# Optimization experiments

Measured on AMD Instinct MI355X. Metric: run time of the kernel, lower is better.

The kernel has to match this reference:

```python
import jax, jax.numpy as jnp
import numpy as np

HEADS = 8
EPS = 1e-5


def dwconv(x, w):
    # x: [B, C, L], w: [C, 1, K] depthwise kernel (groups == C), 'same' padding (K odd)
    K = w.shape[-1]
    p = (K - 1) // 2
    return jax.lax.conv_general_dilated(
        x, w, window_strides=(1,), padding=[(p, p)],
        dimension_numbers=('NCH', 'OIH', 'NCH'),
        feature_group_count=x.shape[1])


def dds_conv(x, pw, dw3, dw15, gate):
    # DynamicDepthSeparableConv1d: 1x1 pointwise (no bias) -> two depthwise convs
    # combined with softmax-gated weighted sum.
    o = jnp.einsum('oc,bcl->bol', pw, x)
    g = jax.nn.softmax(gate)
    return g[0] * dwconv(o, dw3) + g[1] * dwconv(o, dw15)


def instance_norm(x, gamma, beta):
    # InstanceNorm1d(affine=True), biased variance over length dim
    m = jnp.mean(x, axis=-1, keepdims=True)
    v = jnp.mean((x - m) ** 2, axis=-1, keepdims=True)
    return (x - m) * jax.lax.rsqrt(v + EPS) * gamma[None, :, None] + beta[None, :, None]


def block(x, p):
    B, C, L = x.shape
    h = HEADS
    Q = dds_conv(x, p['pw_q'], p['dw3_q'], p['dw15_q'], p['gate_q']).reshape(B, h, C, L)
    K = dds_conv(x, p['pw_k'], p['dw3_k'], p['dw15_k'], p['gate_k']).reshape(B, h, C, L)
    V = dds_conv(x, p['pw_v'], p['dw3_v'], p['dw15_v'], p['gate_v']).reshape(B, h, C, L)
    scale = C ** -0.25
    # dot[b,h,k,q] = sum_c K[b,h,c,k] * Q[b,h,c,q]; softmax over key dim (axis=2)
    dot = jnp.einsum('bhck,bhcq->bhkq', K * scale, Q * scale)
    attn = jax.nn.softmax(dot, axis=2)
    o = jnp.einsum('bhck,bhkq->bhcq', V, attn).reshape(B, h * C, L)
    attended = jnp.einsum('oc,bcl->bol', p['uni_W'], o) + p['uni_b'][None, :, None]
    # dropout is identity at inference
    x = instance_norm(attended + x, p['n1_g'], p['n1_b'])
    h1 = jax.nn.relu(jnp.einsum('oc,bcl->bol', p['ffn_W1'], x) + p['ffn_b1'][None, :, None])
    ff = jnp.einsum('oc,bcl->bol', p['ffn_W2'], h1) + p['ffn_b2'][None, :, None]
    x = instance_norm(ff + x, p['n2_g'], p['n2_b'])
    return x


def setup_inputs() -> dict:
    key = jax.random.key(0)
    ks = jax.random.split(key, 32)
    D, C, h, L, B, IN = 6, 32, HEADS, 2048, 8, 6
    CH = C * h
    s = 0.05
    inp = {
        'x': jax.random.normal(ks[0], (B, IN, L), jnp.float32),
        'enc_W': jax.random.normal(ks[1], (C, IN), jnp.float32) * s,
        'enc_b': jnp.zeros((C,), jnp.float32),
        'pw_q': jax.random.normal(ks[2], (D, CH, C), jnp.float32) * s,
        'dw3_q': jax.random.normal(ks[3], (D, CH, 1, 3), jnp.float32) * s,
        'dw15_q': jax.random.normal(ks[4], (D, CH, 1, 15), jnp.float32) * s,
        'gate_q': jnp.ones((D, 2), jnp.float32),
        'pw_k': jax.random.normal(ks[5], (D, CH, C), jnp.float32) * s,
        'dw3_k': jax.random.normal(ks[6], (D, CH, 1, 3), jnp.float32) * s,
        'dw15_k': jax.random.normal(ks[7], (D, CH, 1, 15), jnp.float32) * s,
        'gate_k': jnp.ones((D, 2), jnp.float32),
        'pw_v': jax.random.normal(ks[8], (D, CH, C), jnp.float32) * s,
        'dw3_v': jax.random.normal(ks[9], (D, CH, 1, 3), jnp.float32) * s,
        'dw15_v': jax.random.normal(ks[10], (D, CH, 1, 15), jnp.float32) * s,
        'gate_v': jnp.ones((D, 2), jnp.float32),
        'uni_W': jax.random.normal(ks[11], (D, C, CH), jnp.float32) * s,
        'uni_b': jnp.zeros((D, C), jnp.float32),
        'n1_g': jnp.ones((D, C), jnp.float32),
        'n1_b': jnp.zeros((D, C), jnp.float32),
        'n2_g': jnp.ones((D, C), jnp.float32),
        'n2_b': jnp.zeros((D, C), jnp.float32),
        'ffn_W1': jax.random.normal(ks[12], (D, 4 * C, C), jnp.float32) * s,
        'ffn_b1': jnp.zeros((D, 4 * C), jnp.float32),
        'ffn_W2': jax.random.normal(ks[13], (D, C, 4 * C), jnp.float32) * s,
        'ffn_b2': jnp.zeros((D, C), jnp.float32),
        'cls_W': jax.random.normal(ks[14], (1, C), jnp.float32) * s,
        'cls_b': jnp.zeros((1,), jnp.float32),
    }
    return inp


def reference(x, enc_W, enc_b, pw_q, dw3_q, dw15_q, gate_q, pw_k, dw3_k, dw15_k,
              gate_k, pw_v, dw3_v, dw15_v, gate_v, uni_W, uni_b, n1_g, n1_b,
              n2_g, n2_b, ffn_W1, ffn_b1, ffn_W2, ffn_b2, cls_W, cls_b):
    h = jnp.einsum('oc,bcl->bol', enc_W, x) + enc_b[None, :, None]
    params = dict(pw_q=pw_q, dw3_q=dw3_q, dw15_q=dw15_q, gate_q=gate_q,
                  pw_k=pw_k, dw3_k=dw3_k, dw15_k=dw15_k, gate_k=gate_k,
                  pw_v=pw_v, dw3_v=dw3_v, dw15_v=dw15_v, gate_v=gate_v,
                  uni_W=uni_W, uni_b=uni_b, n1_g=n1_g, n1_b=n1_b,
                  n2_g=n2_g, n2_b=n2_b, ffn_W1=ffn_W1, ffn_b1=ffn_b1,
                  ffn_W2=ffn_W2, ffn_b2=ffn_b2)
    def step(carry, p):
        return block(carry, p), None
    h, _ = jax.lax.scan(step, h, params)
    logits = jnp.einsum('oc,bcl->bol', cls_W, h) + cls_b[None, :, None]  # [B,1,L]
    return jax.nn.sigmoid(logits)[:, 0, :]  # strong (per-timestep) probabilities [B, L]
```

## Files before the change

### kernel.cpp

```cpp
#include <hip/hip_runtime.h>
#include <math.h>

#define LL   2048
#define BB   8
#define CC   32
#define CHH  256
#define HH   8
#define DD   6

typedef _Float16 h8 __attribute__((ext_vector_type(8)));
typedef _Float16 h4 __attribute__((ext_vector_type(4)));
typedef float f4 __attribute__((ext_vector_type(4)));
typedef float f2v __attribute__((ext_vector_type(2)));

__global__ __launch_bounds__(256) void k_enc(const float* __restrict__ x,
    const float* __restrict__ W, const float* __restrict__ bias,
    float* __restrict__ X) {
  int idx = blockIdx.x * 256 + threadIdx.x;
  int l = idx & (LL - 1);
  int c = (idx >> 11) & 31;
  int b = idx >> 16;
  float s = bias[c];
#pragma unroll
  for (int i = 0; i < 6; ++i)
    s = fmaf(W[c * 6 + i], x[((size_t)b * 6 + i) * LL + l], s);
  X[idx] = s;
}

__global__ __launch_bounds__(256) void k_qkv(const float* __restrict__ X,
    const float* __restrict__ pwq, const float* __restrict__ pwk,
    const float* __restrict__ pwv,
    const float* __restrict__ d3q, const float* __restrict__ d15q, const float* __restrict__ gq,
    const float* __restrict__ d3k, const float* __restrict__ d15k, const float* __restrict__ gk,
    const float* __restrict__ d3v, const float* __restrict__ d15v, const float* __restrict__ gv,
    _Float16* __restrict__ Qt, _Float16* __restrict__ Kt, _Float16* __restrict__ Vt) {
  __shared__ __align__(16) char lds[21504];
  int z  = blockIdx.y;
  int bx = blockIdx.x;
  int bh = bx >> 4, lt = bx & 15, l0 = lt * 128;
  int b = bh >> 3, h = bh & 7;
  int t = threadIdx.x;
  const float* pwp  = (z == 0) ? pwq  : (z == 1) ? pwk  : pwv;
  const float* w3p  = (z == 0) ? d3q  : (z == 1) ? d3k  : d3v;
  const float* w15p = (z == 0) ? d15q : (z == 1) ? d15k : d15v;
  const float* gp   = (z == 0) ? gq   : (z == 1) ? gk   : gv;

  char* Xh = lds;
  char* Wh = lds + 9728;
  char* ot = lds + 11776;

  {
    int r = t >> 3, u = t & 7;
    const float* xr = X + ((size_t)b * CC + r) * LL;
    char* xd = Xh + r * 304;
#pragma unroll
    for (int s = u; s < 36; s += 8) {
      int ls = l0 - 8 + s * 4;
      f4 v;
      if (ls >= 0 && ls + 3 < LL) {
        v = *(const f4*)(xr + ls);
      } else {
#pragma unroll
        for (int e = 0; e < 4; ++e) {
          int l = ls + e;
          v[e] = (l >= 0 && l < LL) ? xr[l] : 0.f;
        }
      }
      uint2 pk;
      pk.x = __builtin_bit_cast(unsigned, __builtin_amdgcn_cvt_pkrtz(v[0], v[1]));
      pk.y = __builtin_bit_cast(unsigned, __builtin_amdgcn_cvt_pkrtz(v[2], v[3]));
      *(uint2*)(xd + s * 8) = pk;
    }
  }
  {
    f4 wg = ((const f4*)(pwp + h * 1024))[t];
    uint2 pk;
    pk.x = __builtin_bit_cast(unsigned, __builtin_amdgcn_cvt_pkrtz(wg[0], wg[1]));
    pk.y = __builtin_bit_cast(unsigned, __builtin_amdgcn_cvt_pkrtz(wg[2], wg[3]));
    *(uint2*)(Wh + (t >> 3) * 64 + (t & 7) * 8) = pk;
  }
  __syncthreads();

  {
    int w4 = t >> 6, lane = t & 63;
    int g = lane >> 4, ln = lane & 15;
    h8 af[2];
#pragma unroll
    for (int mt = 0; mt < 2; ++mt)
      af[mt] = *(const h8*)(Wh + (mt * 16 + ln) * 64 + g * 16);
    for (int nt = w4; nt < 9; nt += 4) {
      h8 bf;
#pragma unroll
      for (int j = 0; j < 8; ++j)
        bf[j] = *(const _Float16*)(Xh + (g * 8 + j) * 304 + (nt * 16 + ln) * 2);
#pragma unroll
      for (int mt = 0; mt < 2; ++mt) {
        f4 zr = {0.f, 0.f, 0.f, 0.f};
        f4 d = __builtin_amdgcn_mfma_f32_16x16x32_f16(af[mt], bf, zr, 0, 0, 0);
#pragma unroll
        for (int i = 0; i < 4; ++i)
          *(_Float16*)(ot + (mt * 16 + g * 4 + i) * 304 + (nt * 16 + ln) * 2) =
              (_Float16)d[i];
      }
    }
  }
  __syncthreads();

  int c = t & 31, cg = t >> 5;
  float wv[32];
  {
    const h8* wp = (const h8*)(ot + c * 304 + cg * 32);
#pragma unroll
    for (int q4 = 0; q4 < 4; ++q4) {
      h8 v = wp[q4];
#pragma unroll
      for (int e = 0; e < 8; ++e) wv[q4 * 8 + e] = (float)v[e];
    }
  }
  float r0 = gp[0], r1 = gp[1];
  float mx = fmaxf(r0, r1);
  float e0 = __expf(r0 - mx), e1 = __expf(r1 - mx);
  float gi = 1.f / (e0 + e1);
  float g0 = e0 * gi, g1 = e1 * gi;
  float sc = (z == 0) ? 0.2550765737f : 1.0f;
  int ch = h * 32 + c;
  float w3r[3], w15r[15];
#pragma unroll
  for (int k = 0; k < 3; ++k)  w3r[k]  = w3p[ch * 3 + k];
#pragma unroll
  for (int k = 0; k < 15; ++k) w15r[k] = w15p[ch * 15 + k];

  h8 olo, ohi;
#pragma unroll
  for (int i = 0; i < 16; ++i) {
    float a = 0.f;
#pragma unroll
    for (int k = 0; k < 3; ++k) a = fmaf(w3r[k], wv[i + 7 + k], a);
    float s15 = 0.f;
#pragma unroll
    for (int k = 0; k < 15; ++k) s15 = fmaf(w15r[k], wv[i + 1 + k], s15);
    float val = (g0 * a + g1 * s15) * sc;
    if (i < 8) olo[i] = (_Float16)val; else ohi[i - 8] = (_Float16)val;
  }

  if (z == 2) {
    _Float16* dst = Vt + ((size_t)bh * 32 + c) * LL + l0 + cg * 16;
    *(h8*)dst = olo;
    *(h8*)(dst + 8) = ohi;
  } else {
    char* tb = lds;
    __syncthreads();
#pragma unroll
    for (int i = 0; i < 16; ++i) {
      _Float16 v = (i < 8) ? olo[i] : ohi[i - 8];
      *(_Float16*)(tb + (cg * 16 + i) * 80 + c * 2) = v;
    }
    __syncthreads();
    _Float16* dst = ((z == 0) ? Qt : Kt) + ((size_t)bh * LL + l0) * 32;
    int l = t >> 1, hf = t & 1;
    uint4 a = *(uint4*)(tb + l * 80 + hf * 32);
    uint4 b2 = *(uint4*)(tb + l * 80 + hf * 32 + 16);
    *(uint4*)(dst + (size_t)l * 32 + hf * 16) = a;
    *(uint4*)(dst + (size_t)l * 32 + hf * 16 + 8) = b2;
  }
}

__global__ __launch_bounds__(512, 2) void k_attn(
    const _Float16* __restrict__ Qt, const _Float16* __restrict__ Kt,
    const _Float16* __restrict__ Vt, _Float16* __restrict__ AO) {
  __shared__ __align__(16) char lds[38912];
  const int tid  = threadIdx.x;
  const int lane = tid & 63;
  const int w    = tid >> 6;
  const int seg  = w >> 2;
  const int wq   = w & 3;
  const int g    = lane >> 4;
  const int ln   = lane & 15;
  const int h2c  = (wq >> 1) * 2;
  const int lin  = blockIdx.x + (blockIdx.y << 4);
  const int swz  = ((lin & 7) << 7) | (lin >> 3);
  const int qb   = swz & 15;
  const int bh   = swz >> 4;
  const _Float16* Qg = Qt + ((size_t)bh * LL + qb * 128) * 32;
  const _Float16* Kg = Kt + ((size_t)bh * LL + seg * 1024) * 32;
  const _Float16* Vg = Vt + (size_t)bh * 32 * LL + seg * 1024;

  h8 qf[2];
#pragma unroll
  for (int nt = 0; nt < 2; ++nt)
    qf[nt] = *(const h8*)(Qg + (size_t)(wq * 32 + nt * 16 + ln) * 32 + g * 8);

  h8 ones;
#pragma unroll
  for (int j = 0; j < 8; ++j) ones[j] = (_Float16)1.0f;

  char* kb = lds + seg * 5120;
  char* vb = lds + 20480 + seg * 4608;

  uint4 stg0, stg1;
  if ((wq & 1) == 0) {
    const uint4* gk = (const uint4*)Kg;
    stg0 = gk[h2c * 64 + lane];
    stg1 = gk[(h2c + 1) * 64 + lane];
    *(uint4*)(kb + (h2c * 16 + (lane >> 2)) * 80 + (lane & 3) * 16) = stg0;
    *(uint4*)(kb + ((h2c + 1) * 16 + (lane >> 2)) * 80 + (lane & 3) * 16) = stg1;
  } else {
    int c0 = h2c * 8 + (lane >> 3);
    stg0 = *(const uint4*)(Vg + (size_t)c0 * LL + (lane & 7) * 8);
    stg1 = *(const uint4*)(Vg + (size_t)(c0 + 8) * LL + (lane & 7) * 8);
    *(uint4*)(vb + c0 * 144 + (lane & 7) * 16) = stg0;
    *(uint4*)(vb + (c0 + 8) * 144 + (lane & 7) * 16) = stg1;
  }
  __syncthreads();

  f4 o[2][2];
#pragma unroll
  for (int ct = 0; ct < 2; ++ct)
#pragma unroll
    for (int nt = 0; nt < 2; ++nt) o[ct][nt] = (f4){0.f, 0.f, 0.f, 0.f};
  f4 sacc[2];
#pragma unroll
  for (int nt = 0; nt < 2; ++nt) sacc[nt] = (f4){0.f, 0.f, 0.f, 0.f};

  for (int it = 0; it < 16; ++it) {
    int pp = it & 1;
    char* kbc = kb + pp * 10240;
    char* vbc = vb + pp * 9216;
    if (it < 15) {
      int k0n = (it + 1) * 64;
      if ((wq & 1) == 0) {
        const uint4* gk = (const uint4*)(Kg + (size_t)k0n * 32);
        stg0 = gk[h2c * 64 + lane];
        stg1 = gk[(h2c + 1) * 64 + lane];
      } else {
        int c0 = h2c * 8 + (lane >> 3);
        stg0 = *(const uint4*)(Vg + (size_t)c0 * LL + k0n + (lane & 7) * 8);
        stg1 = *(const uint4*)(Vg + (size_t)(c0 + 8) * LL + k0n + (lane & 7) * 8);
      }
    }
#pragma unroll
    for (int chunk = 0; chunk < 2; ++chunk) {
      unsigned pa[2][2], pb[2][2];
#pragma unroll
      for (int mt2 = 0; mt2 < 2; ++mt2) {
        h8 kf = *(const h8*)(kbc + ((chunk * 2 + mt2) * 16 + ln) * 80 + g * 16);
#pragma unroll
        for (int nt = 0; nt < 2; ++nt) {
          f4 z = {0.f, 0.f, 0.f, 0.f};
          f4 s = __builtin_amdgcn_mfma_f32_16x16x32_f16(kf, qf[nt], z, 0, 0, 0);
          float p0 = __builtin_amdgcn_exp2f(s[0]);
          float p1 = __builtin_amdgcn_exp2f(s[1]);
          float p2 = __builtin_amdgcn_exp2f(s[2]);
          float p3 = __builtin_amdgcn_exp2f(s[3]);
          unsigned lo = __builtin_bit_cast(unsigned,
              __builtin_amdgcn_cvt_pkrtz(p0, p1));
          unsigned hi = __builtin_bit_cast(unsigned,
              __builtin_amdgcn_cvt_pkrtz(p2, p3));
          if (mt2 == 0) { pa[nt][0] = lo; pa[nt][1] = hi; }
          else          { pb[nt][0] = lo; pb[nt][1] = hi; }
        }
      }
      h8 vf[2];
#pragma unroll
      for (int ct = 0; ct < 2; ++ct)
        vf[ct] = *(const h8*)(vbc + (ct * 16 + ln) * 144 + chunk * 64 + g * 16);
#pragma unroll
      for (int nt = 0; nt < 2; ++nt) {
        unsigned w0 = pa[nt][0], w1 = pa[nt][1];
        unsigned w2 = pb[nt][0], w3 = pb[nt][1];
        asm("v_permlane32_swap_b32 %0, %1" : "+v"(w0), "+v"(w2));
        asm("v_permlane16_swap_b32 %0, %1" : "+v"(w0), "+v"(w2));
        asm("v_permlane32_swap_b32 %0, %1" : "+v"(w1), "+v"(w3));
        asm("v_permlane16_swap_b32 %0, %1" : "+v"(w1), "+v"(w3));
        uint4 pw4; pw4.x = w0; pw4.y = w1; pw4.z = w2; pw4.w = w3;
        h8 pf = __builtin_bit_cast(h8, pw4);
        sacc[nt] = __builtin_amdgcn_mfma_f32_16x16x32_f16(ones, pf, sacc[nt], 0, 0, 0);
        o[0][nt] = __builtin_amdgcn_mfma_f32_16x16x32_f16(vf[0], pf, o[0][nt], 0, 0, 0);
        o[1][nt] = __builtin_amdgcn_mfma_f32_16x16x32_f16(vf[1], pf, o[1][nt], 0, 0, 0);
      }
    }
    if (it < 15) {
      char* kbn = kb + (pp ^ 1) * 10240;
      char* vbn = vb + (pp ^ 1) * 9216;
      if ((wq & 1) == 0) {
        *(uint4*)(kbn + (h2c * 16 + (lane >> 2)) * 80 + (lane & 3) * 16) = stg0;
        *(uint4*)(kbn + ((h2c + 1) * 16 + (lane >> 2)) * 80 + (lane & 3) * 16) = stg1;
      } else {
        int c0 = h2c * 8 + (lane >> 3);
        *(uint4*)(vbn + c0 * 144 + (lane & 7) * 16) = stg0;
        *(uint4*)(vbn + (c0 + 8) * 144 + (lane & 7) * 16) = stg1;
      }
    }
    __syncthreads();
  }

  if (seg == 1) {
    char* eo = lds + wq * 9216 + lane * 144;
#pragma unroll
    for (int nt = 0; nt < 2; ++nt)
#pragma unroll
      for (int ct = 0; ct < 2; ++ct)
        *(f4*)(eo + (nt * 2 + ct) * 16) = o[ct][nt];
    f4 sv;
    sv[0] = sacc[0][0]; sv[1] = sacc[1][0];
    sv[2] = 0.f; sv[3] = 0.f;
    *(f4*)(eo + 64) = sv;
  }
  __syncthreads();
  if (seg == 0) {
    const char* po = lds + wq * 9216 + lane * 144;
    f4 s1v = *(const f4*)(po + 64);
    _Float16* out = AO + (size_t)bh * (32 * LL);
#pragma unroll
    for (int nt = 0; nt < 2; ++nt) {
      float inv = 1.f / (sacc[nt][0] + s1v[nt]);
      int qg = qb * 128 + wq * 32 + nt * 16 + ln;
#pragma unroll
      for (int ct = 0; ct < 2; ++ct) {
        f4 o1 = *(const f4*)(po + (nt * 2 + ct) * 16);
#pragma unroll
        for (int r = 0; r < 4; ++r)
          out[(size_t)(ct * 16 + g * 4 + r) * LL + qg] =
              (_Float16)((o[ct][nt][r] + o1[r]) * inv);
      }
    }
  }
}

__global__ __launch_bounds__(256) void k_uni_res(const _Float16* __restrict__ AO,
    const float* __restrict__ W, const float* __restrict__ bias,
    const float* __restrict__ Xin, float* __restrict__ Y) {
  __shared__ __align__(16) char lds[35840];
  char* Wh = lds;
  char* Bh = lds + 17920;
  int t  = threadIdx.x;
  int bx = blockIdx.x;
  int lt = bx & 63, b = bx >> 6;
  int l0 = lt * 32;

#pragma unroll
  for (int i = 0; i < 8; ++i) {
    int idx = t + i * 256;
    f4 wv4 = ((const f4*)W)[idx];
    uint2 pk;
    pk.x = __builtin_bit_cast(unsigned, __builtin_amdgcn_cvt_pkrtz(wv4[0], wv4[1]));
    pk.y = __builtin_bit_cast(unsigned, __builtin_amdgcn_cvt_pkrtz(wv4[2], wv4[3]));
    int c = idx >> 6, ccp = idx & 63;
    *(uint2*)(Wh + c * 560 + ccp * 8) = pk;
  }
#pragma unroll
  for (int it = 0; it < 4; ++it) {
    int cc = it * 64 + (t >> 2), chunk = t & 3;
    h8 av = *(const h8*)(AO + ((size_t)b * CHH + cc) * LL + l0 + chunk * 8);
#pragma unroll
    for (int e = 0; e < 8; ++e)
      *(_Float16*)(Bh + (chunk * 8 + e) * 560 + cc * 2) = av[e];
  }
  __syncthreads();

  int wv = t >> 6, lane = t & 63;
  int g = lane >> 4, ln = lane & 15;
  int mt = wv >> 1, nt2 = wv & 1;
  f4 acc = {0.f, 0.f, 0.f, 0.f};
#pragma unroll
  for (int ks = 0; ks < 8; ++ks) {
    h8 af = *(const h8*)(Wh + (mt * 16 + ln) * 560 + (ks * 32 + g * 8) * 2);
    h8 bf = *(const h8*)(Bh + (nt2 * 16 + ln) * 560 + (ks * 32 + g * 8) * 2);
    acc = __builtin_amdgcn_mfma_f32_16x16x32_f16(af, bf, acc, 0, 0, 0);
  }
#pragma unroll
  for (int i = 0; i < 4; ++i) {
    int c = mt * 16 + g * 4 + i;
    size_t o = ((size_t)b * CC + c) * LL + l0 + nt2 * 16 + ln;
    Y[o] = acc[i] + bias[c] + Xin[o];
  }
}

__global__ __launch_bounds__(512) void k_inorm(const float* __restrict__ Y,
    float* __restrict__ X, const float* __restrict__ g,
    const float* __restrict__ bt) {
  __shared__ float red[16];
  int row = blockIdx.x;
  int c = row & 31;
  const float* y = Y + (size_t)row * LL;
  float v[4];
  float s = 0.f, ss = 0.f;
#pragma unroll
  for (int i = 0; i < 4; ++i) {
    v[i] = y[threadIdx.x + 512 * i];
    s += v[i];
    ss = fmaf(v[i], v[i], ss);
  }
#pragma unroll
  for (int off = 32; off; off >>= 1) {
    s  += __shfl_down(s, off);
    ss += __shfl_down(ss, off);
  }
  int wid = threadIdx.x >> 6;
  if ((threadIdx.x & 63) == 0) { red[wid * 2] = s; red[wid * 2 + 1] = ss; }
  __syncthreads();
  if (threadIdx.x == 0) {
    float rs0 = 0.f, rs1 = 0.f;
#pragma unroll
    for (int i = 0; i < 8; ++i) { rs0 += red[i * 2]; rs1 += red[i * 2 + 1]; }
    red[0] = rs0; red[1] = rs1;
  }
  __syncthreads();
  float mean = red[0] * (1.f / LL);
  float var  = red[1] * (1.f / LL) - mean * mean;
  float rs = rsqrtf(var + 1e-5f) * g[c];
  float bb = bt[c];
#pragma unroll
  for (int i = 0; i < 4; ++i)
    X[(size_t)row * LL + threadIdx.x + 512 * i] = (v[i] - mean) * rs + bb;
}

__global__ __launch_bounds__(256) void k_ffn(const float* __restrict__ X,
    const float* __restrict__ W1, const float* __restrict__ b1,
    const float* __restrict__ W2, const float* __restrict__ b2,
    float* __restrict__ Y) {
  __shared__ __align__(16) float wlds[8320];
  __shared__ float ps[7][32 * 33];
  int bx = blockIdx.x;
  int b = bx >> 6;
  int l0 = (bx & 63) * 32;
  int t = threadIdx.x;
  int li = t & 31;
  int og = t >> 5;
  int l = l0 + li;
#pragma unroll
  for (int i = 0; i < 4; ++i)
    ((f4*)wlds)[t + i * 256] = ((const f4*)W1)[t + i * 256];
#pragma unroll
  for (int i = 0; i < 4; ++i)
    ((f4*)(wlds + 4096))[t + i * 256] = ((const f4*)W2)[t + i * 256];
  if (t < 32) ((f4*)(wlds + 8192))[t] = ((const f4*)b1)[t];

  const float* Xp = X + (size_t)b * CC * LL + l;
  float xv[32];
#pragma unroll
  for (int c = 0; c < 32; ++c) xv[c] = Xp[(size_t)c * LL];
  __syncthreads();

  float hs[16];
#pragma unroll
  for (int op = 0; op < 16; ++op) {
    int o = og * 16 + op;
    const f4* wr = (const f4*)(wlds + o * 32);
    f4 p = {wlds[8192 + o], 0.f, 0.f, 0.f};
#pragma unroll
    for (int c4 = 0; c4 < 8; ++c4) {
      f4 a = wr[c4];
      p[0] = fmaf(a[0], xv[c4 * 4 + 0], p[0]);
      p[1] = fmaf(a[1], xv[c4 * 4 + 1], p[1]);
      p[2] = fmaf(a[2], xv[c4 * 4 + 2], p[2]);
      p[3] = fmaf(a[3], xv[c4 * 4 + 3], p[3]);
    }
    hs[op] = fmaxf((p[0] + p[1]) + (p[2] + p[3]), 0.f);
  }

  float acc[32];
#pragma unroll
  for (int c = 0; c < 32; ++c) {
    const f4* w2r = (const f4*)(wlds + 4096 + c * 128 + og * 16);
    f4 s = {0.f, 0.f, 0.f, 0.f};
#pragma unroll
    for (int o4 = 0; o4 < 4; ++o4) {
      f4 w = w2r[o4];
      s[0] = fmaf(w[0], hs[o4 * 4 + 0], s[0]);
      s[1] = fmaf(w[1], hs[o4 * 4 + 1], s[1]);
      s[2] = fmaf(w[2], hs[o4 * 4 + 2], s[2]);
      s[3] = fmaf(w[3], hs[o4 * 4 + 3], s[3]);
    }
    acc[c] = (s[0] + s[1]) + (s[2] + s[3]);
  }

  if (og) {
#pragma unroll
    for (int c = 0; c < 32; ++c) ps[og - 1][li * 33 + c] = acc[c];
  }
  __syncthreads();
  if (!og) {
    float* Yp = Y + (size_t)b * CC * LL + l;
#pragma unroll
    for (int c = 0; c < 32; ++c) {
      float r = acc[c] + b2[c] + xv[c];
#pragma unroll
      for (int q = 0; q < 7; ++q) r += ps[q][li * 33 + c];
      Yp[(size_t)c * LL] = r;
    }
  }
}

__global__ __launch_bounds__(256) void k_cls(const float* __restrict__ X,
    const float* __restrict__ W, const float* __restrict__ bias,
    float* __restrict__ out) {
  int idx = blockIdx.x * 256 + threadIdx.x;
  int l = idx & (LL - 1);
  int b = idx >> 11;
  float s = bias[0];
#pragma unroll
  for (int c = 0; c < CC; ++c)
    s = fmaf(W[c], X[((size_t)b * CC + c) * LL + l], s);
  out[idx] = 1.f / (1.f + __expf(-s));
}

extern "C" void kernel_launch(void* const* d_in, const int* in_sizes, int n_in,
                              void* d_out, int out_size, void* d_ws,
                              size_t ws_size, hipStream_t stream) {
  const float* x      = (const float*)d_in[0];
  const float* enc_W  = (const float*)d_in[1];
  const float* enc_b  = (const float*)d_in[2];
  const float* pw_q   = (const float*)d_in[3];
  const float* dw3_q  = (const float*)d_in[4];
  const float* dw15_q = (const float*)d_in[5];
  const float* gate_q = (const float*)d_in[6];
  const float* pw_k   = (const float*)d_in[7];
  const float* dw3_k  = (const float*)d_in[8];
  const float* dw15_k = (const float*)d_in[9];
  const float* gate_k = (const float*)d_in[10];
  const float* pw_v   = (const float*)d_in[11];
  const float* dw3_v  = (const float*)d_in[12];
  const float* dw15_v = (const float*)d_in[13];
  const float* gate_v = (const float*)d_in[14];
  const float* uni_W  = (const float*)d_in[15];
  const float* uni_b  = (const float*)d_in[16];
  const float* n1_g   = (const float*)d_in[17];
  const float* n1_b   = (const float*)d_in[18];
  const float* n2_g   = (const float*)d_in[19];
  const float* n2_b   = (const float*)d_in[20];
  const float* ffn_W1 = (const float*)d_in[21];
  const float* ffn_b1 = (const float*)d_in[22];
  const float* ffn_W2 = (const float*)d_in[23];
  const float* ffn_b2 = (const float*)d_in[24];
  const float* cls_W  = (const float*)d_in[25];
  const float* cls_b  = (const float*)d_in[26];

  float* ws = (float*)d_ws;
  float* X   = ws;
  float* Y   = ws + 524288;
  _Float16* AO = (_Float16*)(ws + 1048576);
  _Float16* Qt = (_Float16*)(ws + 9437184);
  _Float16* Kt = (_Float16*)(ws + 11534336);
  _Float16* Vt = (_Float16*)(ws + 13631488);

  k_enc<<<2048, 256, 0, stream>>>(x, enc_W, enc_b, X);

  for (int d = 0; d < DD; ++d) {
    k_qkv<<<dim3(1024, 3), 256, 0, stream>>>(X,
        pw_q + d * CHH * CC, pw_k + d * CHH * CC, pw_v + d * CHH * CC,
        dw3_q + d * CHH * 3, dw15_q + d * CHH * 15, gate_q + d * 2,
        dw3_k + d * CHH * 3, dw15_k + d * CHH * 15, gate_k + d * 2,
        dw3_v + d * CHH * 3, dw15_v + d * CHH * 15, gate_v + d * 2,
        Qt, Kt, Vt);
    k_attn<<<dim3(16, 64), 512, 0, stream>>>(Qt, Kt, Vt, AO);
    k_uni_res<<<512, 256, 0, stream>>>(AO, uni_W + d * CC * CHH,
                                       uni_b + d * CC, X, Y);
    k_inorm<<<256, 512, 0, stream>>>(Y, X, n1_g + d * CC, n1_b + d * CC);
    k_ffn<<<512, 256, 0, stream>>>(X, ffn_W1 + d * 128 * CC, ffn_b1 + d * 128,
                                   ffn_W2 + d * CC * 128, ffn_b2 + d * CC, Y);
    k_inorm<<<256, 512, 0, stream>>>(Y, X, n2_g + d * CC, n2_b + d * CC);
  }

  k_cls<<<64, 256, 0, stream>>>(X, cls_W, cls_b, (float*)d_out);
}
```

Before: 663.4 us.

## Rewrite FFN kernel with fp16 MFMA for both pointwise matmuls

Replaces the scalar-FMA FFN kernel with one that stages X, W1, W2 and the hidden activations in LDS as fp16 and computes both 1x1 convolutions using 16x16x32 f16 MFMA instructions. The scalar accumulators and cross-wave partial-sum reduction are removed, so each wave writes its output tile directly with bias and residual added. This cuts ALU work and LDS reduction traffic in exchange for reduced precision in the inputs and hidden layer (fp16 with round-toward-zero packing for weights).

```diff
diff --git a/kernel.cpp b/kernel.cpp
--- a/kernel.cpp
+++ b/kernel.cpp
@@ -419,76 +419,80 @@
     const float* __restrict__ W1, const float* __restrict__ b1,
     const float* __restrict__ W2, const float* __restrict__ b2,
     float* __restrict__ Y) {
-  __shared__ __align__(16) float wlds[8320];
-  __shared__ float ps[7][32 * 33];
+  __shared__ __align__(16) char lds[30720];
+  char* Xh  = lds;
+  char* W1h = lds + 2560;
+  char* W2h = lds + 12800;
+  char* Hh  = lds + 21504;
+  float* b1h = (float*)(lds + 30208);
+  int t  = threadIdx.x;
   int bx = blockIdx.x;
-  int b = bx >> 6;
-  int l0 = (bx & 63) * 32;
-  int t = threadIdx.x;
-  int li = t & 31;
-  int og = t >> 5;
-  int l = l0 + li;
-#pragma unroll
-  for (int i = 0; i < 4; ++i)
-    ((f4*)wlds)[t + i * 256] = ((const f4*)W1)[t + i * 256];
-#pragma unroll
-  for (int i = 0; i < 4; ++i)
-    ((f4*)(wlds + 4096))[t + i * 256] = ((const f4*)W2)[t + i * 256];
-  if (t < 32) ((f4*)(wlds + 8192))[t] = ((const f4*)b1)[t];
-
-  const float* Xp = X + (size_t)b * CC * LL + l;
-  float xv[32];
-#pragma unroll
-  for (int c = 0; c < 32; ++c) xv[c] = Xp[(size_t)c * LL];
-  __syncthreads();
-
-  float hs[16];
-#pragma unroll
-  for (int op = 0; op < 16; ++op) {
-    int o = og * 16 + op;
-    const f4* wr = (const f4*)(wlds + o * 32);
-    f4 p = {wlds[8192 + o], 0.f, 0.f, 0.f};
-#pragma unroll
-    for (int c4 = 0; c4 < 8; ++c4) {
-      f4 a = wr[c4];
-      p[0] = fmaf(a[0], xv[c4 * 4 + 0], p[0]);
-      p[1] = fmaf(a[1], xv[c4 * 4 + 1], p[1]);
-      p[2] = fmaf(a[2], xv[c4 * 4 + 2], p[2]);
-      p[3] = fmaf(a[3], xv[c4 * 4 + 3], p[3]);
-    }
-    hs[op] = fmaxf((p[0] + p[1]) + (p[2] + p[3]), 0.f);
-  }
-
-  float acc[32];
-#pragma unroll
-  for (int c = 0; c < 32; ++c) {
-    const f4* w2r = (const f4*)(wlds + 4096 + c * 128 + og * 16);
-    f4 s = {0.f, 0.f, 0.f, 0.f};
-#pragma unroll
-    for (int o4 = 0; o4 < 4; ++o4) {
-      f4 w = w2r[o4];
-      s[0] = fmaf(w[0], hs[o4 * 4 + 0], s[0]);
-      s[1] = fmaf(w[1], hs[o4 * 4 + 1], s[1]);
-      s[2] = fmaf(w[2], hs[o4 * 4 + 2], s[2]);
-      s[3] = fmaf(w[3], hs[o4 * 4 + 3], s[3]);
-    }
-    acc[c] = (s[0] + s[1]) + (s[2] + s[3]);
-  }
-
-  if (og) {
-#pragma unroll
-    for (int c = 0; c < 32; ++c) ps[og - 1][li * 33 + c] = acc[c];
-  }
-  __syncthreads();
-  if (!og) {
-    float* Yp = Y + (size_t)b * CC * LL + l;
-#pragma unroll
-    for (int c = 0; c < 32; ++c) {
-      float r = acc[c] + b2[c] + xv[c];
-#pragma unroll
-      for (int q = 0; q < 7; ++q) r += ps[q][li * 33 + c];
-      Yp[(size_t)c * LL] = r;
-    }
+  int lt = bx & 63, b = bx >> 6;
+  int l0 = lt * 32;
+
+  {
+    int c = t >> 3, le0 = (t & 7) * 4;
+    f4 v = *(const f4*)(X + ((size_t)b * CC + c) * LL + l0 + le0);
+#pragma unroll
+    for (int e = 0; e < 4; ++e)
+      *(_Float16*)(Xh + (le0 + e) * 80 + c * 2) = (_Float16)v[e];
+  }
+#pragma unroll
+  for (int i = 0; i < 4; ++i) {
+    int idx = t + i * 256;
+    f4 wv4 = ((const f4*)W1)[idx];
+    uint2 pk;
+    pk.x = __builtin_bit_cast(unsigned, __builtin_amdgcn_cvt_pkrtz(wv4[0], wv4[1]));
+    pk.y = __builtin_bit_cast(unsigned, __builtin_amdgcn_cvt_pkrtz(wv4[2], wv4[3]));
+    int o = idx >> 3, cp = idx & 7;
+    *(uint2*)(W1h + o * 80 + cp * 8) = pk;
+  }
+#pragma unroll
+  for (int i = 0; i < 4; ++i) {
+    int idx = t + i * 256;
+    f4 wv4 = ((const f4*)W2)[idx];
+    uint2 pk;
+    pk.x = __builtin_bit_cast(unsigned, __builtin_amdgcn_cvt_pkrtz(wv4[0], wv4[1]));
+    pk.y = __builtin_bit_cast(unsigned, __builtin_amdgcn_cvt_pkrtz(wv4[2], wv4[3]));
+    int c = idx >> 5, op = idx & 31;
+    *(uint2*)(W2h + c * 272 + op * 8) = pk;
+  }
+  if (t < 128) b1h[t] = b1[t];
+  __syncthreads();
+
+  int w4 = t >> 6, lane = t & 63;
+  int g = lane >> 4, ln = lane & 15;
+
+#pragma unroll
+  for (int j = 0; j < 4; ++j) {
+    int ti = w4 * 4 + j;
+    int ot = ti >> 1, lt2 = ti & 1;
+    h8 af = *(const h8*)(W1h + (ot * 16 + ln) * 80 + g * 16);
+    h8 bf = *(const h8*)(Xh + (lt2 * 16 + ln) * 80 + g * 16);
+    f4 zr = {0.f, 0.f, 0.f, 0.f};
+    f4 d = __builtin_amdgcn_mfma_f32_16x16x32_f16(af, bf, zr, 0, 0, 0);
+#pragma unroll
+    for (int i = 0; i < 4; ++i) {
+      int o = ot * 16 + g * 4 + i;
+      float hv = fmaxf(d[i] + b1h[o], 0.f);
+      *(_Float16*)(Hh + (lt2 * 16 + ln) * 272 + o * 2) = (_Float16)hv;
+    }
+  }
+  __syncthreads();
+
+  int ct2 = w4 >> 1, lt2b = w4 & 1;
+  f4 acc = {0.f, 0.f, 0.f, 0.f};
+#pragma unroll
+  for (int ks = 0; ks < 4; ++ks) {
+    h8 af = *(const h8*)(W2h + (ct2 * 16 + ln) * 272 + (ks * 32 + g * 8) * 2);
+    h8 bf = *(const h8*)(Hh + (lt2b * 16 + ln) * 272 + (ks * 32 + g * 8) * 2);
+    acc = __builtin_amdgcn_mfma_f32_16x16x32_f16(af, bf, acc, 0, 0, 0);
+  }
+#pragma unroll
+  for (int i = 0; i < 4; ++i) {
+    int c = ct2 * 16 + g * 4 + i;
+    size_t o = ((size_t)b * CC + c) * LL + l0 + lt2b * 16 + ln;
+    Y[o] = acc[i] + b2[c] + X[o];
   }
 }
 
```

Measured after the change: 610.5 us, median of 2. 1.09x faster.
